# Performance work log

Hardware: AMD Instinct MI355X
Metric: run time of the kernel (lower is better)

## Reference

```python
import jax, jax.numpy as jnp
import numpy as np

N_HID = 4
EPS = 1e-6  # LayerNorm eps (note: added to std, torch-style, std with ddof=1)


def _rnn_layer(wx_out, prev_pre, uh, g, b):
    """Sequential recurrence: at = wx_out[k] + h @ Uh^T; skip-subtract prev pre-act;
    custom layernorm (gamma*(x-mean)/(std+eps)+beta, std unbiased); relu.
    Returns (hiddens [T,B,H], pre_acts [T,B,H])."""
    T, B, H = wx_out.shape

    def step(h, inp):
        wx_k, prev_k = inp
        at = wx_k + h @ uh.T          # [B,H]
        pre = at
        a = at - prev_k               # skip connection (subtract prev layer pre-act)
        mean = a.mean(-1, keepdims=True)
        std = jnp.std(a, axis=-1, ddof=1, keepdims=True)
        a = g * (a - mean) / (std + EPS) + b
        h_new = jax.nn.relu(a)        # drop_mask = 1-drop_rate = 1.0 (test mode, drop_rate=0)
        return h_new, (h_new, pre)

    h0 = jnp.zeros((B, H), wx_out.dtype)
    _, (hs, pres) = jax.lax.scan(step, h0, (wx_out, prev_pre))
    return hs, pres


def setup_inputs() -> dict:
    key = jax.random.key(0)
    ks = jax.random.split(key, 12)
    T, B, D, H, C = 400, 32, 440, 1024, 3500
    s = 0.02
    return {
        "x": jax.random.normal(ks[0], (T, B, D), dtype=jnp.float32),
        "lab": jax.random.randint(ks[1], (T, B), 0, C),
        "test_flag": 1,
        "wx0_w": jax.random.normal(ks[2], (H, D), dtype=jnp.float32) * s,
        "wx0_b": jnp.zeros((H,), jnp.float32),
        "wx_w": jax.random.normal(ks[3], (N_HID - 1, H, H), dtype=jnp.float32) * s,
        "wx_b": jnp.zeros((N_HID - 1, H), jnp.float32),
        "uh_w": jax.random.normal(ks[4], (N_HID, H, H), dtype=jnp.float32) * s,
        "ln_g": jnp.ones((N_HID, H), jnp.float32),
        "ln_b": jnp.zeros((N_HID, H), jnp.float32),
        "fco_w": jax.random.normal(ks[5], (C, H), dtype=jnp.float32) * s,
        "fco_b": jnp.zeros((C,), jnp.float32),
    }


def reference(x, lab, test_flag, wx0_w, wx0_b, wx_w, wx_b, uh_w, ln_g, ln_b, fco_w, fco_b):
    T, B, _ = x.shape
    H = uh_w.shape[-1]
    prev_pre = jnp.zeros((T, B, H), x.dtype)  # skip_conn: layer 0 subtracts zeros
    h = x
    for i in range(N_HID):
        if i == 0:
            wx_out = jnp.einsum('tbd,hd->tbh', h, wx0_w) + wx0_b
        else:
            wx_out = jnp.einsum('tbd,hd->tbh', h, wx_w[i - 1]) + wx_b[i - 1]
        h, prev_pre = _rnn_layer(wx_out, prev_pre, uh_w[i], ln_g[i], ln_b[i])
    out = jnp.einsum('tbh,ch->tbc', h, fco_w) + fco_b   # [T,B,C]
    pout = jax.nn.log_softmax(out, axis=2)
    pred = jnp.argmax(pout, axis=2)
    nll = -jnp.take_along_axis(pout, lab[..., None], axis=2).squeeze(-1)
    loss = nll.mean()
    err = jnp.mean((pred != lab).astype(jnp.float32))
    return loss, err, pout
```

## Files before the change

### kernel.cpp

```cpp
#include <hip/hip_runtime.h>
#include <math.h>

#define T_STEPS 400
#define BATCH   32
#define HID     1024
#define MROWS   (T_STEPS * BATCH)
#define NCLS    3500
#define NG      8
#define BPG     4
#define CPG     32
#define JS      32
#define EPS     1e-6f
#define SLOTP   8

typedef __attribute__((ext_vector_type(8))) short short8v;
typedef __attribute__((ext_vector_type(4))) float f32x4;

__device__ __forceinline__ unsigned short bf16_rne(float x) {
  unsigned u = __builtin_bit_cast(unsigned, x);
  unsigned r = u + 0x7FFFu + ((u >> 16) & 1u);
  return (unsigned short)(r >> 16);
}

__device__ __forceinline__ void stage_tile(
    const float* __restrict__ src, int rowlim, int row0, int ld,
    int k0, int K, unsigned short* hi, unsigned short* lo, int tid) {
  #pragma unroll
  for (int it = 0; it < 2; ++it) {
    const int task = tid + 256 * it;
    const int r = task >> 2, q = task & 3;
    const int gr = row0 + r;
    const bool rok = gr < rowlim;
    const float* p = src + (size_t)gr * ld + k0 + q * 8;
    float x[8];
    if (rok && (k0 + 32 <= K)) {
      float4 v0 = *(const float4*)p;
      float4 v1 = *(const float4*)(p + 4);
      x[0] = v0.x; x[1] = v0.y; x[2] = v0.z; x[3] = v0.w;
      x[4] = v1.x; x[5] = v1.y; x[6] = v1.z; x[7] = v1.w;
    } else {
      #pragma unroll
      for (int j = 0; j < 8; ++j)
        x[j] = (rok && (k0 + q * 8 + j) < K) ? p[j] : 0.f;
    }
    unsigned hp[4], lp[4];
    #pragma unroll
    for (int j = 0; j < 4; ++j) {
      unsigned short h0 = bf16_rne(x[2 * j]), h1 = bf16_rne(x[2 * j + 1]);
      float f0 = __builtin_bit_cast(float, (unsigned)h0 << 16);
      float f1 = __builtin_bit_cast(float, (unsigned)h1 << 16);
      unsigned short l0 = bf16_rne(x[2 * j] - f0), l1 = bf16_rne(x[2 * j + 1] - f1);
      hp[j] = (unsigned)h0 | ((unsigned)h1 << 16);
      lp[j] = (unsigned)l0 | ((unsigned)l1 << 16);
    }
    const int idx = (r * 4 + (q ^ (r & 3))) * 8;
    *(uint4*)&hi[idx] = make_uint4(hp[0], hp[1], hp[2], hp[3]);
    *(uint4*)&lo[idx] = make_uint4(lp[0], lp[1], lp[2], lp[3]);
  }
}

template <int NPASS>
__global__ __launch_bounds__(256) void gemm_mfma(
    const float* __restrict__ A, const float* __restrict__ W,
    const float* __restrict__ bias, float* __restrict__ C,
    int M, int N, int K) {
  __shared__ unsigned short Ah[128 * 32], Al[128 * 32];
  __shared__ unsigned short Bh[128 * 32], Bl[128 * 32];
  const int tid = threadIdx.x;
  const int m0 = blockIdx.y * 128, n0 = blockIdx.x * 128;
  const int w = tid >> 6, lane = tid & 63;
  const int rlow = lane & 15, ksel = lane >> 4;

  f32x4 acc[8][2];
  #pragma unroll
  for (int i = 0; i < 8; ++i) {
    acc[i][0] = (f32x4)(0.f);
    acc[i][1] = (f32x4)(0.f);
  }

  for (int k0 = 0; k0 < K; k0 += 32) {
    __syncthreads();
    stage_tile(A, M, m0, K, k0, K, Ah, Al, tid);
    stage_tile(W, N, n0, K, k0, K, Bh, Bl, tid);
    __syncthreads();

    short8v wh[2], wl[2];
    #pragma unroll
    for (int nf = 0; nf < 2; ++nf) {
      const int rn = w * 32 + nf * 16 + rlow;
      const int idx = (rn * 4 + (ksel ^ (rn & 3))) * 8;
      wh[nf] = *(const short8v*)&Bh[idx];
      if (NPASS == 3) wl[nf] = *(const short8v*)&Bl[idx];
    }
    #pragma unroll
    for (int i = 0; i < 8; ++i) {
      const int ra = i * 16 + rlow;
      const int idx = (ra * 4 + (ksel ^ (ra & 3))) * 8;
      short8v ah = *(const short8v*)&Ah[idx];
      if (NPASS == 3) {
        short8v al = *(const short8v*)&Al[idx];
        acc[i][0] = __builtin_amdgcn_mfma_f32_16x16x32_bf16(ah, wh[0], acc[i][0], 0, 0, 0);
        acc[i][0] = __builtin_amdgcn_mfma_f32_16x16x32_bf16(al, wh[0], acc[i][0], 0, 0, 0);
        acc[i][0] = __builtin_amdgcn_mfma_f32_16x16x32_bf16(ah, wl[0], acc[i][0], 0, 0, 0);
        acc[i][1] = __builtin_amdgcn_mfma_f32_16x16x32_bf16(ah, wh[1], acc[i][1], 0, 0, 0);
        acc[i][1] = __builtin_amdgcn_mfma_f32_16x16x32_bf16(al, wh[1], acc[i][1], 0, 0, 0);
        acc[i][1] = __builtin_amdgcn_mfma_f32_16x16x32_bf16(ah, wl[1], acc[i][1], 0, 0, 0);
      } else {
        acc[i][0] = __builtin_amdgcn_mfma_f32_16x16x32_bf16(ah, wh[0], acc[i][0], 0, 0, 0);
        acc[i][1] = __builtin_amdgcn_mfma_f32_16x16x32_bf16(ah, wh[1], acc[i][1], 0, 0, 0);
      }
    }
  }

  int col[2]; float bb[2]; bool cok[2];
  #pragma unroll
  for (int nf = 0; nf < 2; ++nf) {
    col[nf] = n0 + w * 32 + nf * 16 + rlow;
    cok[nf] = col[nf] < N;
    bb[nf] = cok[nf] ? bias[col[nf]] : 0.f;
  }
  #pragma unroll
  for (int i = 0; i < 8; ++i) {
    const int row = m0 + i * 16 + ksel * 4;
    #pragma unroll
    for (int nf = 0; nf < 2; ++nf) {
      if (cok[nf]) {
        float* cp = C + (size_t)row * N + col[nf];
        cp[0 * N] = acc[i][nf][0] + bb[nf];
        cp[1 * N] = acc[i][nf][1] + bb[nf];
        cp[2 * N] = acc[i][nf][2] + bb[nf];
        cp[3 * N] = acc[i][nf][3] + bb[nf];
      }
    }
  }
}

__global__ void transpose1024(const float* __restrict__ in, float* __restrict__ out) {
  __shared__ float tile[32][33];
  const int bx = blockIdx.x * 32, by = blockIdx.y * 32;
  const int tx = threadIdx.x, ty = threadIdx.y;
  #pragma unroll
  for (int i = 0; i < 32; i += 8)
    tile[ty + i][tx] = in[(size_t)(by + ty + i) * HID + bx + tx];
  __syncthreads();
  #pragma unroll
  for (int i = 0; i < 32; i += 8)
    out[(size_t)(bx + ty + i) * HID + by + tx] = tile[tx][ty + i];
}

__global__ __launch_bounds__(256, 1) void scan_layer(
    const float* __restrict__ wx, const float* __restrict__ uhT,
    float* __restrict__ h_all, float* __restrict__ pre_all,
    float* __restrict__ a_pub,
    int* __restrict__ prog,
    const float* __restrict__ gamma, const float* __restrict__ beta,
    int skip_sub) {
  const int tid  = threadIdx.x;
  const int g    = blockIdx.x >> 5;
  const int c    = blockIdx.x & 31;
  const int lane = tid & 63;
  const int wv   = tid >> 6;
  const int jw   = tid & 3;
  const int ks   = tid >> 2;
  const int col0 = c * JS + jw * 8;

  int* prog_g = prog + (size_t)g * CPG * SLOTP;

  __shared__ float h_lds[HID * BPG];
  __shared__ float a_lds[BPG * HID];
  __shared__ float partial[4][BPG][JS];
  __shared__ float stats_lds[BPG][2];
  __shared__ float g_lds[HID], be_lds[HID];

  for (int k = tid; k < HID; k += 256) { g_lds[k] = gamma[k]; be_lds[k] = beta[k]; }

  float4 u0[16], u1[16];
  #pragma unroll
  for (int i = 0; i < 16; ++i) {
    const float* p = uhT + (size_t)(ks + 64 * i) * HID + col0;
    u0[i] = *(const float4*)p;
    u1[i] = *(const float4*)(p + 4);
  }
  __syncthreads();

  for (int t = 0; t < T_STEPS; ++t) {
    const int par = t & 1;
    float* apub_t = a_pub + ((size_t)par * NG + g) * (BPG * HID);

    float at0 = 0.f, pre_old = 0.f;
    size_t gidx = 0;
    if (tid < 128) {
      const int b = tid >> 5, j = tid & 31;
      gidx = ((size_t)t * BATCH + g * BPG + b) * HID + c * JS + j;
      at0 = wx[gidx];
      pre_old = skip_sub ? 0.f : pre_all[gidx];
    }

    if (t > 0) {
      float pacc[4][8];
      #pragma unroll
      for (int b = 0; b < 4; ++b)
        #pragma unroll
        for (int q = 0; q < 8; ++q) pacc[b][q] = 0.f;
      #pragma unroll
      for (int i = 0; i < 16; ++i) {
        float4 h4 = *(const float4*)&h_lds[(ks + 64 * i) * 4];
        #pragma unroll
        for (int b = 0; b < 4; ++b) {
          float hb = ((const float*)&h4)[b];
          pacc[b][0] += hb * u0[i].x; pacc[b][1] += hb * u0[i].y;
          pacc[b][2] += hb * u0[i].z; pacc[b][3] += hb * u0[i].w;
          pacc[b][4] += hb * u1[i].x; pacc[b][5] += hb * u1[i].y;
          pacc[b][6] += hb * u1[i].z; pacc[b][7] += hb * u1[i].w;
        }
      }
      #pragma unroll
      for (int b = 0; b < 4; ++b)
        #pragma unroll
        for (int q = 0; q < 8; ++q) {
          float v = pacc[b][q];
          v += __shfl_xor(v, 4);
          v += __shfl_xor(v, 8);
          v += __shfl_xor(v, 16);
          v += __shfl_xor(v, 32);
          pacc[b][q] = v;
        }
      if ((lane >> 2) == 0) {
        #pragma unroll
        for (int b = 0; b < 4; ++b) {
          *(float4*)&partial[wv][b][jw * 8]     = *(const float4*)&pacc[b][0];
          *(float4*)&partial[wv][b][jw * 8 + 4] = *(const float4*)&pacc[b][4];
        }
      }
    }
    __syncthreads();

    if (tid < 128) {
      const int b = tid >> 5, j = tid & 31;
      float red = 0.f;
      if (t > 0)
        red = partial[0][b][j] + partial[1][b][j] + partial[2][b][j] + partial[3][b][j];
      float at = at0 + red;
      pre_all[gidx] = at;
      __hip_atomic_store(&apub_t[(size_t)b * HID + c * JS + j], at - pre_old,
                         __ATOMIC_RELAXED, __HIP_MEMORY_SCOPE_AGENT);
    }
    asm volatile("s_waitcnt vmcnt(0)" ::: "memory");
    __syncthreads();

    if (tid == 0)
      __hip_atomic_store(&prog_g[c * SLOTP], t + 1,
                         __ATOMIC_RELAXED, __HIP_MEMORY_SCOPE_AGENT);
    if (wv == 0) {
      const int* p = &prog_g[(lane & 31) * SLOTP];
      while (true) {
        int v = __hip_atomic_load(p, __ATOMIC_RELAXED, __HIP_MEMORY_SCOPE_AGENT);
        if (__all(v >= t + 1)) break;
        __builtin_amdgcn_s_sleep(1);
      }
    }
    __syncthreads();

    {
      float tmp[16];
      #pragma unroll
      for (int j = 0; j < 16; ++j)
        tmp[j] = __hip_atomic_load(&apub_t[tid + 256 * j],
                                   __ATOMIC_RELAXED, __HIP_MEMORY_SCOPE_AGENT);
      #pragma unroll
      for (int j = 0; j < 16; ++j)
        a_lds[tid + 256 * j] = tmp[j];
    }
    __syncthreads();

    {
      float s1 = 0.f, s2 = 0.f;
      #pragma unroll
      for (int i = 0; i < 16; ++i) {
        float v = a_lds[wv * HID + i * 64 + lane];
        s1 += v; s2 += v * v;
      }
      #pragma unroll
      for (int m = 1; m <= 32; m <<= 1) { s1 += __shfl_xor(s1, m); s2 += __shfl_xor(s2, m); }
      if (lane == 0) {
        float mean = s1 * (1.f / HID);
        float var = (s2 - (float)HID * mean * mean) * (1.f / (float)(HID - 1));
        stats_lds[wv][0] = mean;
        stats_lds[wv][1] = sqrtf(fmaxf(var, 0.f)) + EPS;
      }
    }
    __syncthreads();

    {
      float mean0 = stats_lds[0][0], rd0 = 1.f / stats_lds[0][1];
      float mean1 = stats_lds[1][0], rd1 = 1.f / stats_lds[1][1];
      float mean2 = stats_lds[2][0], rd2 = 1.f / stats_lds[2][1];
      float mean3 = stats_lds[3][0], rd3 = 1.f / stats_lds[3][1];
      #pragma unroll
      for (int j = 0; j < 4; ++j) {
        const int k = tid + 256 * j;
        float gk = g_lds[k], bk = be_lds[k];
        float h0 = fmaxf(gk * (a_lds[0 * HID + k] - mean0) * rd0 + bk, 0.f);
        float h1 = fmaxf(gk * (a_lds[1 * HID + k] - mean1) * rd1 + bk, 0.f);
        float h2 = fmaxf(gk * (a_lds[2 * HID + k] - mean2) * rd2 + bk, 0.f);
        float h3 = fmaxf(gk * (a_lds[3 * HID + k] - mean3) * rd3 + bk, 0.f);
        *(float4*)&h_lds[k * 4] = make_float4(h0, h1, h2, h3);
        if (c == 0) {
          h_all[((size_t)t * BATCH + g * BPG + 0) * HID + k] = h0;
          h_all[((size_t)t * BATCH + g * BPG + 1) * HID + k] = h1;
          h_all[((size_t)t * BATCH + g * BPG + 2) * HID + k] = h2;
          h_all[((size_t)t * BATCH + g * BPG + 3) * HID + k] = h3;
        }
      }
    }
    __syncthreads();
  }
}

__global__ __launch_bounds__(256) void softmax_loss(
    float* __restrict__ out, const int* __restrict__ lab, float* __restrict__ acc) {
  __shared__ float rowbuf[NCLS];
  __shared__ float rv[4]; __shared__ int ri[4]; __shared__ float rs[4];
  __shared__ float shv[2];
  __shared__ int shidx;
  const int m = blockIdx.x;
  float* row = out + (size_t)m * NCLS;
  const int tid = threadIdx.x;
  const int lane = tid & 63, wid = tid >> 6;

  float vmax = -1e30f; int vidx = 0x7fffffff;
  for (int c = tid; c < NCLS; c += 256) {
    float v = row[c];
    rowbuf[c] = v;
    if (v > vmax) { vmax = v; vidx = c; }
  }
  #pragma unroll
  for (int off = 32; off; off >>= 1) {
    float ov = __shfl_down(vmax, off);
    int oi = __shfl_down(vidx, off);
    if (ov > vmax || (ov == vmax && oi < vidx)) { vmax = ov; vidx = oi; }
  }
  if (lane == 0) { rv[wid] = vmax; ri[wid] = vidx; }
  __syncthreads();
  if (tid == 0) {
    float bm = rv[0]; int bi = ri[0];
    for (int w = 1; w < 4; ++w)
      if (rv[w] > bm || (rv[w] == bm && ri[w] < bi)) { bm = rv[w]; bi = ri[w]; }
    shv[0] = bm; shidx = bi;
  }
  __syncthreads();
  float gmax = shv[0];
  float s = 0.f;
  for (int c = tid; c < NCLS; c += 256) s += expf(rowbuf[c] - gmax);
  #pragma unroll
  for (int off = 32; off; off >>= 1) s += __shfl_down(s, off);
  if (lane == 0) rs[wid] = s;
  __syncthreads();
  if (tid == 0) shv[1] = rs[0] + rs[1] + rs[2] + rs[3];
  __syncthreads();
  float lse = logf(shv[1]);
  for (int c = tid; c < NCLS; c += 256) row[c] = rowbuf[c] - gmax - lse;
  if (tid == 0) {
    int lb = lab[m];
    float nll = -(rowbuf[lb] - gmax - lse);
    atomicAdd(acc + 0, nll);
    atomicAdd(acc + 1, (shidx != lb) ? 1.f : 0.f);
  }
}

__global__ void init_acc(float* acc) { acc[threadIdx.x] = 0.f; }

__global__ void finalize_out(const float* __restrict__ acc, float* __restrict__ out) {
  out[0] = acc[0] * (1.f / (float)MROWS);
  out[1] = acc[1] * (1.f / (float)MROWS);
}

extern "C" void kernel_launch(void* const* d_in, const int* in_sizes, int n_in,
                              void* d_out, int out_size, void* d_ws, size_t ws_size,
                              hipStream_t stream) {
  const float* x     = (const float*)d_in[0];
  const int*   lab   = (const int*)d_in[1];
  const float* wx0_w = (const float*)d_in[3];
  const float* wx0_b = (const float*)d_in[4];
  const float* wx_w  = (const float*)d_in[5];
  const float* wx_b  = (const float*)d_in[6];
  const float* uh_w  = (const float*)d_in[7];
  const float* ln_g  = (const float*)d_in[8];
  const float* ln_b  = (const float*)d_in[9];
  const float* fco_w = (const float*)d_in[10];
  const float* fco_b = (const float*)d_in[11];
  float* out = (float*)d_out;

  float* wsf = (float*)d_ws;
  size_t off = 0;
  auto carve = [&](size_t n) { float* p = wsf + off; off += (n + 63) & ~(size_t)63; return p; };
  float* uhT   = carve((size_t)HID * HID);
  float* wxbuf = carve((size_t)MROWS * HID);
  float* h_all = carve((size_t)MROWS * HID);
  float* pre   = carve((size_t)MROWS * HID);
  float* a_pub = carve((size_t)2 * NG * BPG * HID);
  int*   prog  = (int*)carve((size_t)4 * NG * CPG * SLOTP);
  float* acc   = carve(64);

  (void)hipMemsetAsync(prog, 0, (size_t)4 * NG * CPG * SLOTP * sizeof(int), stream);
  init_acc<<<1, 2, 0, stream>>>(acc);

  for (int layer = 0; layer < 4; ++layer) {
    if (layer == 0) {
      gemm_mfma<3><<<dim3(HID / 128, MROWS / 128), 256, 0, stream>>>(
          x, wx0_w, wx0_b, wxbuf, MROWS, HID, 440);
    } else {
      gemm_mfma<3><<<dim3(HID / 128, MROWS / 128), 256, 0, stream>>>(
          h_all, wx_w + (size_t)(layer - 1) * HID * HID,
          wx_b + (size_t)(layer - 1) * HID, wxbuf, MROWS, HID, HID);
    }
    transpose1024<<<dim3(32, 32), dim3(32, 8), 0, stream>>>(
        uh_w + (size_t)layer * HID * HID, uhT);

    scan_layer<<<dim3(NG * CPG), 256, 0, stream>>>(
        wxbuf, uhT, h_all, pre, a_pub, prog + (size_t)layer * NG * CPG * SLOTP,
        ln_g + (size_t)layer * HID, ln_b + (size_t)layer * HID,
        (layer == 0) ? 1 : 0);
  }

  gemm_mfma<1><<<dim3((NCLS + 127) / 128, MROWS / 128), 256, 0, stream>>>(
      h_all, fco_w, fco_b, out + 2, MROWS, NCLS, HID);
  softmax_loss<<<MROWS, 256, 0, stream>>>(out + 2, lab, acc);
  finalize_out<<<1, 1, 0, stream>>>(acc, out);
}
```

Before: 10.06 ms.

## Replace progress-counter barrier with step-tagged 64-bit data exchange in scan

Each published activation value is now packed with its step number into a 64-bit word. Readers poll the data slots directly until the tags match, so the separate progress counters, the memory-fence wait and two block barriers per step are gone. Blocks are also remapped so that the members of a batch group come from interleaved block IDs (g = blockIdx & 7), which likely places each group on one XCD so the exchange stays within a shared cache. The cost is double the bytes in the exchange buffer and per-element polling traffic. The buffer is no longer zeroed, so correctness relies on stale tags never matching the wanted step.

```diff
diff --git a/kernel.cpp b/kernel.cpp
--- a/kernel.cpp
+++ b/kernel.cpp
@@ -11,7 +11,6 @@
 #define CPG     32
 #define JS      32
 #define EPS     1e-6f
-#define SLOTP   8
 
 typedef __attribute__((ext_vector_type(8))) short short8v;
 typedef __attribute__((ext_vector_type(4))) float f32x4;
@@ -151,21 +150,18 @@
 __global__ __launch_bounds__(256, 1) void scan_layer(
     const float* __restrict__ wx, const float* __restrict__ uhT,
     float* __restrict__ h_all, float* __restrict__ pre_all,
-    float* __restrict__ a_pub,
-    int* __restrict__ prog,
+    unsigned long long* __restrict__ a_pub,
     const float* __restrict__ gamma, const float* __restrict__ beta,
     int skip_sub) {
   const int tid  = threadIdx.x;
-  const int g    = blockIdx.x >> 5;
-  const int c    = blockIdx.x & 31;
+  const int g    = blockIdx.x & 7;
+  const int c    = blockIdx.x >> 3;
   const int lane = tid & 63;
   const int wv   = tid >> 6;
   const int jw   = tid & 3;
   const int ks   = tid >> 2;
   const int col0 = c * JS + jw * 8;
 
-  int* prog_g = prog + (size_t)g * CPG * SLOTP;
-
   __shared__ float h_lds[HID * BPG];
   __shared__ float a_lds[BPG * HID];
   __shared__ float partial[4][BPG][JS];
@@ -185,7 +181,7 @@
 
   for (int t = 0; t < T_STEPS; ++t) {
     const int par = t & 1;
-    float* apub_t = a_pub + ((size_t)par * NG + g) * (BPG * HID);
+    unsigned long long* apub_t = a_pub + ((size_t)par * NG + g) * (BPG * HID);
 
     float at0 = 0.f, pre_old = 0.f;
     size_t gidx = 0;
@@ -242,34 +238,39 @@
         red = partial[0][b][j] + partial[1][b][j] + partial[2][b][j] + partial[3][b][j];
       float at = at0 + red;
       pre_all[gidx] = at;
-      __hip_atomic_store(&apub_t[(size_t)b * HID + c * JS + j], at - pre_old,
+      float av = at - pre_old;
+      unsigned long long pk =
+          ((unsigned long long)(unsigned)(t + 1) << 32) |
+          (unsigned long long)__builtin_bit_cast(unsigned, av);
+      __hip_atomic_store(&apub_t[(size_t)b * HID + c * JS + j], pk,
                          __ATOMIC_RELAXED, __HIP_MEMORY_SCOPE_AGENT);
     }
-    asm volatile("s_waitcnt vmcnt(0)" ::: "memory");
-    __syncthreads();
-
-    if (tid == 0)
-      __hip_atomic_store(&prog_g[c * SLOTP], t + 1,
-                         __ATOMIC_RELAXED, __HIP_MEMORY_SCOPE_AGENT);
-    if (wv == 0) {
-      const int* p = &prog_g[(lane & 31) * SLOTP];
-      while (true) {
-        int v = __hip_atomic_load(p, __ATOMIC_RELAXED, __HIP_MEMORY_SCOPE_AGENT);
-        if (__all(v >= t + 1)) break;
-        __builtin_amdgcn_s_sleep(1);
-      }
-    }
-    __syncthreads();
 
     {
-      float tmp[16];
-      #pragma unroll
-      for (int j = 0; j < 16; ++j)
-        tmp[j] = __hip_atomic_load(&apub_t[tid + 256 * j],
-                                   __ATOMIC_RELAXED, __HIP_MEMORY_SCOPE_AGENT);
-      #pragma unroll
-      for (int j = 0; j < 16; ++j)
-        a_lds[tid + 256 * j] = tmp[j];
+      const unsigned wanted = (unsigned)(t + 1);
+      unsigned pend = 0xFFFFu;
+      float vals[16];
+      while (pend) {
+        #pragma unroll
+        for (int s = 0; s < 16; ++s) {
+          if (pend & (1u << s)) {
+            const int b = s >> 2, j = s & 3;
+            unsigned long long pk = __hip_atomic_load(
+                &apub_t[(size_t)b * HID + tid + 256 * j],
+                __ATOMIC_RELAXED, __HIP_MEMORY_SCOPE_AGENT);
+            if ((unsigned)(pk >> 32) == wanted) {
+              vals[s] = __builtin_bit_cast(float, (unsigned)pk);
+              pend &= ~(1u << s);
+            }
+          }
+        }
+        if (pend) __builtin_amdgcn_s_sleep(1);
+      }
+      #pragma unroll
+      for (int s = 0; s < 16; ++s) {
+        const int b = s >> 2, j = s & 3;
+        a_lds[b * HID + tid + 256 * j] = vals[s];
+      }
     }
     __syncthreads();
 
@@ -398,11 +399,10 @@
   float* wxbuf = carve((size_t)MROWS * HID);
   float* h_all = carve((size_t)MROWS * HID);
   float* pre   = carve((size_t)MROWS * HID);
-  float* a_pub = carve((size_t)2 * NG * BPG * HID);
-  int*   prog  = (int*)carve((size_t)4 * NG * CPG * SLOTP);
+  unsigned long long* a_pub =
+      (unsigned long long*)carve((size_t)2 * 2 * NG * BPG * HID);
   float* acc   = carve(64);
 
-  (void)hipMemsetAsync(prog, 0, (size_t)4 * NG * CPG * SLOTP * sizeof(int), stream);
   init_acc<<<1, 2, 0, stream>>>(acc);
 
   for (int layer = 0; layer < 4; ++layer) {
@@ -418,7 +418,7 @@
         uh_w + (size_t)layer * HID * HID, uhT);
 
     scan_layer<<<dim3(NG * CPG), 256, 0, stream>>>(
-        wxbuf, uhT, h_all, pre, a_pub, prog + (size_t)layer * NG * CPG * SLOTP,
+        wxbuf, uhT, h_all, pre, a_pub,
         ln_g + (size_t)layer * HID, ln_b + (size_t)layer * HID,
         (layer == 0) ? 1 : 0);
   }
```

New measurement: 14.33 ms. 1.42x slower.
